# Performance work log

Measured on AMD Instinct MI355X. Metric: run time of the kernel, lower is better.

Reference implementation:

```python
import jax, jax.numpy as jnp
import numpy as np
from jax import lax

B, L = 128, 26          # batch, sequence length (25-iteration loop => L = 26)
C1, C2 = 128, 64        # conv channel widths (n_filters)
K1, K2 = 7, 5           # conv kernel sizes
N_POS = 25              # hardcoded position loop in original module
H = 1 + L * C2 + (C2 * C2) * (N_POS * (N_POS + 1) // 2)  # 1332865


def setup_inputs() -> dict:
    key = jax.random.key(0)
    ks = jax.random.split(key, 6)
    x = jax.random.randint(ks[0], (B, L), 0, 4)                      # nucleotide ids 0..3
    conv1_w = jax.random.normal(ks[1], (C1, 4, K1), jnp.float32) * 0.1
    conv1_b = jnp.zeros((C1,), jnp.float32)
    conv2_w = jax.random.normal(ks[2], (C2, C1, K2), jnp.float32) * 0.05
    conv2_b = jnp.zeros((C2,), jnp.float32)
    reg_w = jax.random.normal(ks[3], (1, H), jnp.float32) * 0.001
    reg_b = jnp.zeros((1,), jnp.float32)
    return {"x": x, "conv1_w": conv1_w, "conv1_b": conv1_b,
            "conv2_w": conv2_w, "conv2_b": conv2_b,
            "reg_w": reg_w, "reg_b": reg_b}


def _conv1d_same_relu(h, w, b):
    # torch Conv1d(padding=k//2) + ReLU; dropout p=0.0 is identity (eval)
    k = w.shape[-1]
    y = lax.conv_general_dilated(h, w, (1,), [(k // 2, k // 2)],
                                 dimension_numbers=('NCH', 'OIH', 'NCH'))
    return jax.nn.relu(y + b[None, :, None])


def reference(x, conv1_w, conv1_b, conv2_w, conv2_b, reg_w, reg_b):
    # one_hot(x).transpose(1,2) -> [B, 4, L]
    h = jax.nn.one_hot(x, 4, dtype=jnp.float32).transpose(0, 2, 1)
    h = _conv1d_same_relu(h, conv1_w, conv1_b)   # [B, C1, L]
    h = _conv1d_same_relu(h, conv2_w, conv2_b)   # [B, C2, L]
    # permute(0,2,1).reshape(B, -1): position-major, channel-minor flat features
    feat = h.transpose(0, 2, 1).reshape(h.shape[0], -1)  # [B, L*C2]
    # pairwise quadratic expansion: for position i, channel j -> feat[:, i*C+j] * feat[:, (i+1)*C:]
    # vectorized per-position as an outer product; 25-iteration structural loop only
    parts = []
    for i in range(N_POS):
        a = feat[:, i * C2:(i + 1) * C2]          # [B, C2]
        b = feat[:, (i + 1) * C2:]                # [B, (L-1-i)*C2]
        parts.append((a[:, :, None] * b[:, None, :]).reshape(feat.shape[0], -1))
    x_second_order = jnp.concatenate(parts, axis=1)       # [B, 325*C2^2]
    full = jnp.concatenate(
        [jnp.ones((feat.shape[0], 1), jnp.float32), feat, x_second_order], axis=1)  # [B, H]
    out = full @ reg_w[0] + reg_b[0]              # Linear(H, 1) -> squeeze -> [B]
    return out
```

## Files before the change

kernel.cpp:

```cpp
#include <hip/hip_runtime.h>

#define B_   128
#define L_   26
#define C1_  128
#define C2_  64
#define K1_  7
#define K2_  5
#define NPOS 25
#define FEAT (L_*C2_)
#define NPAIR (NPOS*(NPOS+1)/2)

__global__ __launch_bounds__(256) void conv_kernel(
    const int*   __restrict__ x,
    const float* __restrict__ w1, const float* __restrict__ b1,
    const float* __restrict__ w2, const float* __restrict__ b2,
    float* __restrict__ featT)
{
    __shared__ float h1s[C1_][L_ + 4];
    __shared__ float w2s[16*C1_*K2_];
    __shared__ int   xs[L_];

    const int bid = blockIdx.x;
    const int b   = bid >> 2;
    const int c2t = bid & 3;
    const int t   = threadIdx.x;

    if (t < L_)  xs[t] = x[b*L_ + t];
    if (t < C1_) { h1s[t][0] = 0.f; h1s[t][1] = 0.f;
                   h1s[t][L_+2] = 0.f; h1s[t][L_+3] = 0.f; }

    {
        const float* src = w2 + c2t*16*C1_*K2_;
        #pragma unroll
        for (int i = 0; i < 10; ++i) {
            const int idx = t*4 + i*1024;
            *(float4*)&w2s[idx] = *(const float4*)&src[idx];
        }
    }
    __syncthreads();

    for (int idx = t; idx < C1_*L_; idx += 256) {
        const int c1 = idx / L_;
        const int l  = idx - c1*L_;
        float s = b1[c1];
        const float* w1r = w1 + c1*4*K1_;
        #pragma unroll
        for (int k = 0; k < K1_; ++k) {
            const int pos = l + k - 3;
            if (pos >= 0 && pos < L_) s += w1r[xs[pos]*K1_ + k];
        }
        h1s[c1][l+2] = fmaxf(s, 0.f);
    }
    __syncthreads();

    for (int o = t; o < 16*L_; o += 256) {
        const int l   = o % L_;
        const int c2i = o / L_;
        const int c2  = c2t*16 + c2i;
        float acc0 = b2[c2], acc1 = 0.f;
        const float* wbase = &w2s[c2i*C1_*K2_];
        for (int c1 = 0; c1 < C1_; c1 += 2) {
            const float* wr0 = wbase + c1*K2_;
            const float* hr0 = &h1s[c1][l];
            acc0 += wr0[0]*hr0[0] + wr0[1]*hr0[1] + wr0[2]*hr0[2]
                  + wr0[3]*hr0[3] + wr0[4]*hr0[4];
            const float* wr1 = wr0 + K2_;
            const float* hr1 = &h1s[c1+1][l];
            acc1 += wr1[0]*hr1[0] + wr1[1]*hr1[1] + wr1[2]*hr1[2]
                  + wr1[3]*hr1[3] + wr1[4]*hr1[4];
        }
        featT[(l*C2_ + c2)*B_ + b] = fmaxf(acc0 + acc1, 0.f);
    }
}

__global__ __launch_bounds__(512) void reg_kernel(
    const float* __restrict__ featT,
    const float* __restrict__ rw, const float* __restrict__ rb,
    float* __restrict__ out)
{
    __shared__ float ws[64*64];
    __shared__ float red[B_];
    const int t = threadIdx.x;
    const int b = t & 127;
    const int quarter = t >> 7;
    const int bid = blockIdx.x;

    if (t < B_) red[t] = 0.f;

    float acc = 0.f;

    if (bid == NPAIR) {
        __syncthreads();
        const int u0 = quarter * (FEAT/4);
        for (int u = u0; u < u0 + FEAT/4; ++u)
            acc += featT[u*B_ + b] * rw[1 + u];
        if (quarter == 0) acc += rw[0] + rb[0];
    } else {
        int i = 0, r = bid;
        while (r >= NPOS - i) { r -= NPOS - i; ++i; }
        const int j = i + 1 + r;

        const int stride = (NPOS - i) * 64;
        const int base   = 1 + FEAT + 4096*(NPOS*i - (i*(i-1))/2)
                         + (j - i - 1)*64;

        #pragma unroll
        for (int k = 0; k < 8; ++k) {
            const int idx = t + k*512;
            ws[idx] = rw[base + (idx >> 6)*stride + (idx & 63)];
        }
        __syncthreads();

        float fj[64];
        #pragma unroll
        for (int q = 0; q < 64; ++q)
            fj[q] = featT[(j*64 + q)*B_ + b];

        const int p0 = quarter * 16;
        float fi[16];
        #pragma unroll
        for (int p = 0; p < 16; ++p)
            fi[p] = featT[(i*64 + p0 + p)*B_ + b];

        #pragma unroll 4
        for (int p = 0; p < 16; ++p) {
            const float4* wrow = (const float4*)&ws[(p0 + p)*64];
            float s0 = 0.f, s1 = 0.f, s2 = 0.f, s3 = 0.f;
            #pragma unroll
            for (int qq = 0; qq < 16; ++qq) {
                const float4 w = wrow[qq];
                s0 += w.x*fj[qq*4+0];
                s1 += w.y*fj[qq*4+1];
                s2 += w.z*fj[qq*4+2];
                s3 += w.w*fj[qq*4+3];
            }
            acc += fi[p] * ((s0+s1)+(s2+s3));
        }
    }

    atomicAdd(&red[b], acc);
    __syncthreads();
    if (t < B_) atomicAdd(&out[t], red[t]);
}

extern "C" void kernel_launch(void* const* d_in, const int* in_sizes, int n_in,
                              void* d_out, int out_size, void* d_ws, size_t ws_size,
                              hipStream_t stream)
{
    const int*   x  = (const int*)  d_in[0];
    const float* w1 = (const float*)d_in[1];
    const float* b1 = (const float*)d_in[2];
    const float* w2 = (const float*)d_in[3];
    const float* b2 = (const float*)d_in[4];
    const float* rw = (const float*)d_in[5];
    const float* rb = (const float*)d_in[6];
    float* out   = (float*)d_out;
    float* featT = (float*)d_ws;

    hipMemsetAsync(out, 0, B_*sizeof(float), stream);
    conv_kernel<<<dim3(512), dim3(256), 0, stream>>>(x, w1, b1, w2, b2, featT);
    reg_kernel <<<dim3(NPAIR+1), dim3(512), 0, stream>>>(featT, rw, rb, out);
}
```

Before: 125.4 us.

## Restructure conv layout, store features batch-major, and shard output reduction

The conv kernel now caches conv1 weights in shared memory and transposes conv2 weights and activations to a channel-contiguous layout. Each thread computes two output positions with float4 loads. Features are stored batch-major so the regression kernel can fetch them as float4 vectors. Final atomics are spread over 16 slices and summed by an extra small kernel, which is meant to cut contention on the 128 output addresses. The cost is one more launch, and the batch-major reads are no longer coalesced across threads.

```diff
diff --git a/kernel.cpp b/kernel.cpp
--- a/kernel.cpp
+++ b/kernel.cpp
@@ -9,6 +9,10 @@
 #define NPOS 25
 #define FEAT (L_*C2_)
 #define NPAIR (NPOS*(NPOS+1)/2)
+#define NSLICE 16
+
+#define HROW 132
+#define WROW 644
 
 __global__ __launch_bounds__(256) void conv_kernel(
     const int*   __restrict__ x,
@@ -16,8 +20,9 @@
     const float* __restrict__ w2, const float* __restrict__ b2,
     float* __restrict__ featT)
 {
-    __shared__ float h1s[C1_][L_ + 4];
-    __shared__ float w2s[16*C1_*K2_];
+    __shared__ float h1s[30*HROW];
+    __shared__ float w2s[16*WROW];
+    __shared__ float w1s[C1_*4*K1_];
     __shared__ int   xs[L_];
 
     const int bid = blockIdx.x;
@@ -25,58 +30,70 @@
     const int c2t = bid & 3;
     const int t   = threadIdx.x;
 
-    if (t < L_)  xs[t] = x[b*L_ + t];
-    if (t < C1_) { h1s[t][0] = 0.f; h1s[t][1] = 0.f;
-                   h1s[t][L_+2] = 0.f; h1s[t][L_+3] = 0.f; }
+    if (t < L_) xs[t] = x[b*L_ + t];
+    if (t < HROW) { h1s[0*HROW+t] = 0.f; h1s[1*HROW+t] = 0.f;
+                    h1s[28*HROW+t] = 0.f; h1s[29*HROW+t] = 0.f; }
+
+    for (int i = t; i < C1_*4*K1_; i += 256) w1s[i] = w1[i];
 
     {
         const float* src = w2 + c2t*16*C1_*K2_;
-        #pragma unroll
-        for (int i = 0; i < 10; ++i) {
-            const int idx = t*4 + i*1024;
-            *(float4*)&w2s[idx] = *(const float4*)&src[idx];
+        for (int idx = t; idx < 16*C1_*K2_; idx += 256) {
+            const int c2i = idx / (C1_*K2_);
+            const int rem = idx - c2i*(C1_*K2_);
+            const int c1  = rem / K2_;
+            const int k   = rem - c1*K2_;
+            w2s[c2i*WROW + k*C1_ + c1] = src[idx];
         }
     }
     __syncthreads();
 
     for (int idx = t; idx < C1_*L_; idx += 256) {
-        const int c1 = idx / L_;
-        const int l  = idx - c1*L_;
+        const int c1 = idx & 127;
+        const int l  = idx >> 7;
         float s = b1[c1];
-        const float* w1r = w1 + c1*4*K1_;
+        const float* w1r = &w1s[c1*4*K1_];
         #pragma unroll
         for (int k = 0; k < K1_; ++k) {
             const int pos = l + k - 3;
             if (pos >= 0 && pos < L_) s += w1r[xs[pos]*K1_ + k];
         }
-        h1s[c1][l+2] = fmaxf(s, 0.f);
+        h1s[(l+2)*HROW + c1] = fmaxf(s, 0.f);
     }
     __syncthreads();
 
-    for (int o = t; o < 16*L_; o += 256) {
-        const int l   = o % L_;
-        const int c2i = o / L_;
-        const int c2  = c2t*16 + c2i;
-        float acc0 = b2[c2], acc1 = 0.f;
-        const float* wbase = &w2s[c2i*C1_*K2_];
-        for (int c1 = 0; c1 < C1_; c1 += 2) {
-            const float* wr0 = wbase + c1*K2_;
-            const float* hr0 = &h1s[c1][l];
-            acc0 += wr0[0]*hr0[0] + wr0[1]*hr0[1] + wr0[2]*hr0[2]
-                  + wr0[3]*hr0[3] + wr0[4]*hr0[4];
-            const float* wr1 = wr0 + K2_;
-            const float* hr1 = &h1s[c1+1][l];
-            acc1 += wr1[0]*hr1[0] + wr1[1]*hr1[1] + wr1[2]*hr1[2]
-                  + wr1[3]*hr1[3] + wr1[4]*hr1[4];
-        }
-        featT[(l*C2_ + c2)*B_ + b] = fmaxf(acc0 + acc1, 0.f);
+    if (t < 16*13) {
+        const int c2i = t & 15;
+        const int lg  = t >> 4;
+        const int l0  = 2*lg, l1 = 2*lg + 1;
+        float a0 = 0.f, a1 = 0.f, a2 = 0.f, a3 = 0.f;
+        #pragma unroll
+        for (int k = 0; k < K2_; ++k) {
+            const float4* wrow = (const float4*)&w2s[c2i*WROW + k*C1_];
+            const float4* h0r  = (const float4*)&h1s[(l0 + k)*HROW];
+            const float4* h1r  = (const float4*)&h1s[(l1 + k)*HROW];
+            #pragma unroll
+            for (int cq = 0; cq < 32; cq += 2) {
+                const float4 w0 = wrow[cq],  w1v = wrow[cq+1];
+                const float4 x0 = h0r[cq],   x1 = h0r[cq+1];
+                const float4 y0 = h1r[cq],   y1 = h1r[cq+1];
+                a0 += w0.x*x0.x + w0.y*x0.y + w0.z*x0.z + w0.w*x0.w;
+                a1 += w1v.x*x1.x + w1v.y*x1.y + w1v.z*x1.z + w1v.w*x1.w;
+                a2 += w0.x*y0.x + w0.y*y0.y + w0.z*y0.z + w0.w*y0.w;
+                a3 += w1v.x*y1.x + w1v.y*y1.y + w1v.z*y1.z + w1v.w*y1.w;
+            }
+        }
+        const int   c2  = c2t*16 + c2i;
+        const float bb  = b2[c2];
+        featT[b*FEAT + l0*C2_ + c2] = fmaxf(a0 + a1 + bb, 0.f);
+        featT[b*FEAT + l1*C2_ + c2] = fmaxf(a2 + a3 + bb, 0.f);
     }
 }
 
 __global__ __launch_bounds__(512) void reg_kernel(
     const float* __restrict__ featT,
     const float* __restrict__ rw, const float* __restrict__ rb,
-    float* __restrict__ out)
+    float* __restrict__ redbuf)
 {
     __shared__ float ws[64*64];
     __shared__ float red[B_];
@@ -92,8 +109,12 @@
     if (bid == NPAIR) {
         __syncthreads();
         const int u0 = quarter * (FEAT/4);
-        for (int u = u0; u < u0 + FEAT/4; ++u)
-            acc += featT[u*B_ + b] * rw[1 + u];
+        const float4* fp = (const float4*)&featT[b*FEAT + u0];
+        for (int q = 0; q < FEAT/16; ++q) {
+            const float4 f = fp[q];
+            const int u = u0 + q*4;
+            acc += f.x*rw[1+u] + f.y*rw[2+u] + f.z*rw[3+u] + f.w*rw[4+u];
+        }
         if (quarter == 0) acc += rw[0] + rb[0];
     } else {
         int i = 0, r = bid;
@@ -111,36 +132,50 @@
         }
         __syncthreads();
 
-        float fj[64];
-        #pragma unroll
-        for (int q = 0; q < 64; ++q)
-            fj[q] = featT[(j*64 + q)*B_ + b];
+        float4 fj[16];
+        const float4* fjp = (const float4*)&featT[b*FEAT + j*64];
+        #pragma unroll
+        for (int q = 0; q < 16; ++q) fj[q] = fjp[q];
 
         const int p0 = quarter * 16;
-        float fi[16];
-        #pragma unroll
-        for (int p = 0; p < 16; ++p)
-            fi[p] = featT[(i*64 + p0 + p)*B_ + b];
-
-        #pragma unroll 4
-        for (int p = 0; p < 16; ++p) {
-            const float4* wrow = (const float4*)&ws[(p0 + p)*64];
-            float s0 = 0.f, s1 = 0.f, s2 = 0.f, s3 = 0.f;
+        const float4* fip = (const float4*)&featT[b*FEAT + i*64 + p0];
+
+        #pragma unroll
+        for (int pq = 0; pq < 4; ++pq) {
+            const float4 f = fip[pq];
+            const float fiv[4] = {f.x, f.y, f.z, f.w};
             #pragma unroll
-            for (int qq = 0; qq < 16; ++qq) {
-                const float4 w = wrow[qq];
-                s0 += w.x*fj[qq*4+0];
-                s1 += w.y*fj[qq*4+1];
-                s2 += w.z*fj[qq*4+2];
-                s3 += w.w*fj[qq*4+3];
+            for (int pp = 0; pp < 4; ++pp) {
+                const int p = p0 + pq*4 + pp;
+                const float4* wrow = (const float4*)&ws[p*64];
+                float s0 = 0.f, s1 = 0.f, s2 = 0.f, s3 = 0.f;
+                #pragma unroll
+                for (int qq = 0; qq < 16; ++qq) {
+                    const float4 w = wrow[qq];
+                    s0 += w.x*fj[qq].x;
+                    s1 += w.y*fj[qq].y;
+                    s2 += w.z*fj[qq].z;
+                    s3 += w.w*fj[qq].w;
+                }
+                acc += fiv[pp] * ((s0+s1)+(s2+s3));
             }
-            acc += fi[p] * ((s0+s1)+(s2+s3));
         }
     }
 
     atomicAdd(&red[b], acc);
     __syncthreads();
-    if (t < B_) atomicAdd(&out[t], red[t]);
+    if (t < B_)
+        atomicAdd(&redbuf[(bid & (NSLICE-1))*B_ + t], red[t]);
+}
+
+__global__ __launch_bounds__(128) void fin_kernel(
+    const float* __restrict__ redbuf, float* __restrict__ out)
+{
+    const int b = threadIdx.x;
+    float s = 0.f;
+    #pragma unroll
+    for (int sl = 0; sl < NSLICE; ++sl) s += redbuf[sl*B_ + b];
+    out[b] = s;
 }
 
 extern "C" void kernel_launch(void* const* d_in, const int* in_sizes, int n_in,
@@ -154,10 +189,12 @@
     const float* b2 = (const float*)d_in[4];
     const float* rw = (const float*)d_in[5];
     const float* rb = (const float*)d_in[6];
-    float* out   = (float*)d_out;
-    float* featT = (float*)d_ws;
-
-    hipMemsetAsync(out, 0, B_*sizeof(float), stream);
+    float* out    = (float*)d_out;
+    float* featT  = (float*)d_ws;
+    float* redbuf = (float*)((char*)d_ws + 851968);
+
+    hipMemsetAsync(redbuf, 0, NSLICE*B_*sizeof(float), stream);
     conv_kernel<<<dim3(512), dim3(256), 0, stream>>>(x, w1, b1, w2, b2, featT);
-    reg_kernel <<<dim3(NPAIR+1), dim3(512), 0, stream>>>(featT, rw, rb, out);
-}
+    reg_kernel <<<dim3(NPAIR+1), dim3(512), 0, stream>>>(featT, rw, rb, redbuf);
+    fin_kernel <<<dim3(1), dim3(128), 0, stream>>>(redbuf, out);
+}
```

New measurement: 131.4 us. 4.8% more time.
